# Performance work log

Measured on AMD Instinct MI355X. Metric: run time of the kernel, lower is better.

## Reference

```python
import jax, jax.numpy as jnp
import numpy as np

B, N, DIM = 1, 2048, 2048
H, KVH = 32, 4                 # query heads, kv heads
D = DIM // H                   # head_dim = 64
REP = H // KVH                 # queries per kv = 8
KV_DIM = D * KVH               # 256


def _rope_tables(n, d, base=10000.0):
    inv = 1.0 / (base ** (np.arange(0, d, 2, dtype=np.float32) / d))
    t = np.arange(n, dtype=np.float32)
    freqs = np.outer(t, inv)                      # [n, d/2]
    emb = np.concatenate([freqs, freqs], axis=-1)  # [n, d]
    return jnp.asarray(np.cos(emb)), jnp.asarray(np.sin(emb))


def setup_inputs() -> dict:
    key = jax.random.key(0)
    ks = jax.random.split(key, 5)
    s = 0.02
    cos, sin = _rope_tables(N, D)
    return {
        "x": jax.random.normal(ks[0], (B, N, DIM), jnp.float32),
        "Wq": jax.random.normal(ks[1], (DIM, DIM), jnp.float32) * s,
        "Wk": jax.random.normal(ks[2], (KV_DIM, DIM), jnp.float32) * s,
        "Wv": jax.random.normal(ks[3], (KV_DIM, DIM), jnp.float32) * s,
        "Wo": jax.random.normal(ks[4], (DIM, DIM), jnp.float32) * s,
        "cos": cos,
        "sin": sin,
    }


def _rotate_half(t):
    d2 = t.shape[-1] // 2
    return jnp.concatenate([-t[..., d2:], t[..., :d2]], axis=-1)


def reference(x, Wq, Wk, Wv, Wo, cos, sin):
    b, n, _ = x.shape
    # projections (nn.Linear: x @ W.T)
    q = (x @ Wq.T).reshape(b, n, H, D).transpose(0, 2, 1, 3)     # b h n d
    k = (x @ Wk.T).reshape(b, n, KVH, D).transpose(0, 2, 1, 3)   # b g n d
    v = (x @ Wv.T).reshape(b, n, KVH, D).transpose(0, 2, 1, 3)
    # RoPE
    c = cos[None, None, :, :]
    s = sin[None, None, :, :]
    q = q * c + _rotate_half(q) * s
    k = k * c + _rotate_half(k) * s
    # expand KV heads (repeat_interleave over head dim)
    k = jnp.repeat(k, REP, axis=1)   # b h n d
    v = jnp.repeat(v, REP, axis=1)
    # causal attention with materialized scores (faithful to source)
    scale = 1.0 / jnp.sqrt(jnp.asarray(D, x.dtype))
    scores = jnp.einsum('bhld,bhsd->bhls', q, k) * scale
    causal = jnp.tril(jnp.ones((n, n), bool))
    scores = jnp.where(causal[None, None], scores, jnp.asarray(-jnp.inf, x.dtype))
    attn = jax.nn.softmax(scores, axis=-1)
    y = jnp.einsum('bhls,bhsd->bhld', attn, v)       # b h n d
    y = y.transpose(0, 2, 1, 3).reshape(b, n, DIM)   # b n (h d)
    return y @ Wo.T
```

## Files before the change

kernel.cpp:

```cpp
#include <hip/hip_runtime.h>

typedef unsigned short u16;
typedef __attribute__((ext_vector_type(8))) short short8;
typedef __attribute__((ext_vector_type(4))) float floatx4;

#define N_TOK 2048
#define DIM   2048
#define NH    32
#define NKVH  4
#define HD    64
#define KVD   256

__device__ __forceinline__ float bf2f(u16 u) {
  union { unsigned i; float f; } c; c.i = ((unsigned)u) << 16; return c.f;
}
__device__ __forceinline__ u16 f2bf(float f) {
  union { float f; unsigned i; } c; c.f = f;
  unsigned x = c.i;
  return (u16)((x + 0x7fffu + ((x >> 16) & 1u)) >> 16);
}

__device__ __forceinline__ void gload16(const u16* g, u16* l) {
#if defined(__has_builtin) && __has_builtin(__builtin_amdgcn_global_load_lds)
  __builtin_amdgcn_global_load_lds(
      (const __attribute__((address_space(1))) void*)g,
      (__attribute__((address_space(3))) void*)l, 16, 0, 0);
#else
  *(short8*)l = *(const short8*)g;
#endif
}

#define C_X  1048576
#define C_WQ 2097152
#define C_WK 2228224
#define C_WV 2359296
#define C_WO 3407872
__global__ __launch_bounds__(256) void cvt_all(const float* __restrict__ x,
                                               const float* __restrict__ wq,
                                               const float* __restrict__ wk,
                                               const float* __restrict__ wv,
                                               const float* __restrict__ wo,
                                               u16* __restrict__ dst) {
  int i = blockIdx.x * 256 + threadIdx.x;
  const float* src; int off;
  if      (i < C_X)  { src = x;  off = 0; }
  else if (i < C_WQ) { src = wq; off = C_X; }
  else if (i < C_WK) { src = wk; off = C_WQ; }
  else if (i < C_WV) { src = wv; off = C_WK; }
  else               { src = wo; off = C_WV; }
  float4 v = ((const float4*)src)[i - off];
  ushort4 o;
  o.x = f2bf(v.x); o.y = f2bf(v.y); o.z = f2bf(v.z); o.w = f2bf(v.w);
  ((ushort4*)dst)[i] = o;
}


__global__ __launch_bounds__(256) void gemm_qkv(const u16* __restrict__ A,
                                                const u16* __restrict__ Wq,
                                                const u16* __restrict__ Wk,
                                                const u16* __restrict__ Wv,
                                                const float* __restrict__ cs,
                                                const float* __restrict__ sn,
                                                u16* __restrict__ Qp,
                                                u16* __restrict__ Kp,
                                                u16* __restrict__ Vp) {
  __shared__ __align__(16) u16 As[64 * 32];
  __shared__ __align__(16) u16 Bs[128 * 32];
  const int tid  = threadIdx.x;
  const int lane = tid & 63;
  const int w    = tid >> 6;
  const int r    = lane & 15, q = lane >> 4;
  const int tm = blockIdx.x & 31;
  const int tn = blockIdx.x >> 5;
  const int wm = w & 1, wn = w >> 1;
  const int K = DIM;

  const u16* W; int wrow0;
  if (tn < 16)      { W = Wq; wrow0 = tn * 128; }
  else if (tn < 18) { W = Wk; wrow0 = (tn - 16) * 128; }
  else              { W = Wv; wrow0 = (tn - 18) * 128; }

  const int srow = tid >> 2;
  const int scol = (tid & 3) * 8;
  const u16* ga = A + (size_t)(tm * 64 + srow) * K + scol;
  const u16* gb = W + (size_t)(wrow0 + srow) * K + scol;
  u16* lA = &As[tid * 8];
  u16* lB = &Bs[tid * 8];

  floatx4 acc[2][4];
#pragma unroll
  for (int a = 0; a < 2; ++a)
#pragma unroll
    for (int b = 0; b < 4; ++b) acc[a][b] = (floatx4){0.f, 0.f, 0.f, 0.f};

  for (int k0 = 0; k0 < K; k0 += 32) {
    __syncthreads();
    gload16(ga + k0, lA);
    gload16(gb + k0, lB);
    gload16(gb + k0 + (size_t)64 * K, lB + 2048);
    __syncthreads();

    short8 af[2], bf[4];
#pragma unroll
    for (int mi = 0; mi < 2; ++mi)
      af[mi] = *(const short8*)&As[(wm * 32 + mi * 16 + r) * 32 + q * 8];
#pragma unroll
    for (int nj = 0; nj < 4; ++nj)
      bf[nj] = *(const short8*)&Bs[(wn * 64 + nj * 16 + r) * 32 + q * 8];
#pragma unroll
    for (int mi = 0; mi < 2; ++mi)
#pragma unroll
      for (int nj = 0; nj < 4; ++nj)
        acc[mi][nj] = __builtin_amdgcn_mfma_f32_16x16x32_bf16(af[mi], bf[nj], acc[mi][nj], 0, 0, 0);
  }

  if (tn < 18) {
    const int head = (tn < 16) ? (tn * 2 + wn) : ((tn - 16) * 2 + wn);
#pragma unroll
    for (int mi = 0; mi < 2; ++mi)
#pragma unroll
      for (int g = 0; g < 4; ++g) {
        int row = tm * 64 + wm * 32 + mi * 16 + 4 * q + g;
        const float* crow  = cs + (size_t)row * 64;
        const float* srow2 = sn + (size_t)row * 64;
#pragma unroll
        for (int nj = 0; nj < 2; ++nj) {
          int d = nj * 16 + r;
          float x0 = acc[mi][nj][g];
          float x1 = acc[mi][nj + 2][g];
          float o0 = x0 * crow[d]      - x1 * srow2[d];
          float o1 = x1 * crow[d + 32] + x0 * srow2[d + 32];
          int qq = d >> 3, j = d & 7;
          int lslot = (qq * 16 + (row & 15)) * 8 + j;
          if (tn < 16) {
            int sq = row >> 5, ii = (row >> 4) & 1;
            size_t base = ((size_t)(head * 64 + sq) * 4 + ii * 2) * 512 + lslot;
            Qp[base]       = f2bf(o0);
            Qp[base + 512] = f2bf(o1);
          } else {
            int kt = row >> 6, t = (row >> 4) & 3;
            size_t base = ((size_t)(head * 32 + kt) * 8 + t * 2) * 512 + lslot;
            Kp[base]       = f2bf(o0);
            Kp[base + 512] = f2bf(o1);
          }
        }
      }
  } else {
#pragma unroll
    for (int mi = 0; mi < 2; ++mi)
#pragma unroll
      for (int nj = 0; nj < 4; ++nj) {
        int col  = (tn - 18) * 128 + wn * 64 + nj * 16 + r;
        int kvh  = col >> 6;
        int t    = (col & 63) >> 4;
        int rr   = col & 15;
        int row0 = tm * 64 + wm * 32 + mi * 16 + 4 * q;
        int kt   = row0 >> 6;
        int wk   = row0 & 63;
        int s    = wk >> 5;
        int qq   = (wk & 31) >> 3;
        int j0   = wk & 7;
        uint2 pk;
        pk.x = (unsigned)f2bf(acc[mi][nj][0]) | ((unsigned)f2bf(acc[mi][nj][1]) << 16);
        pk.y = (unsigned)f2bf(acc[mi][nj][2]) | ((unsigned)f2bf(acc[mi][nj][3]) << 16);
        size_t idx = ((size_t)(kvh * 32 + kt) * 8 + s * 4 + t) * 512 + (qq * 16 + rr) * 8 + j0;
        *(uint2*)(Vp + idx) = pk;
      }
  }
}

__global__ __launch_bounds__(256) void gemm_out(const u16* __restrict__ A,
                                                const u16* __restrict__ W,
                                                float* __restrict__ C) {
  __shared__ __align__(16) u16 As[64 * 32];
  __shared__ __align__(16) u16 Bs[128 * 32];
  const int tid  = threadIdx.x;
  const int lane = tid & 63;
  const int w    = tid >> 6;
  const int r    = lane & 15, q = lane >> 4;
  const int tn = blockIdx.x & 15;
  const int tm = blockIdx.x >> 4;
  const int wm = w & 1, wn = w >> 1;
  const int K = DIM;

  const int srow = tid >> 2;
  const int scol = (tid & 3) * 8;
  const u16* ga = A + (size_t)(tm * 64 + srow) * K + scol;
  const u16* gb = W + (size_t)(tn * 128 + srow) * K + scol;
  u16* lA = &As[tid * 8];
  u16* lB = &Bs[tid * 8];

  floatx4 acc[2][4];
#pragma unroll
  for (int a = 0; a < 2; ++a)
#pragma unroll
    for (int b = 0; b < 4; ++b) acc[a][b] = (floatx4){0.f, 0.f, 0.f, 0.f};

  for (int k0 = 0; k0 < K; k0 += 32) {
    __syncthreads();
    gload16(ga + k0, lA);
    gload16(gb + k0, lB);
    gload16(gb + k0 + (size_t)64 * K, lB + 2048);
    __syncthreads();

    short8 af[2], bf[4];
#pragma unroll
    for (int mi = 0; mi < 2; ++mi)
      af[mi] = *(const short8*)&As[(wm * 32 + mi * 16 + r) * 32 + q * 8];
#pragma unroll
    for (int nj = 0; nj < 4; ++nj)
      bf[nj] = *(const short8*)&Bs[(wn * 64 + nj * 16 + r) * 32 + q * 8];
#pragma unroll
    for (int mi = 0; mi < 2; ++mi)
#pragma unroll
      for (int nj = 0; nj < 4; ++nj)
        acc[mi][nj] = __builtin_amdgcn_mfma_f32_16x16x32_bf16(af[mi], bf[nj], acc[mi][nj], 0, 0, 0);
  }

#pragma unroll
  for (int mi = 0; mi < 2; ++mi)
#pragma unroll
    for (int g = 0; g < 4; ++g) {
      int row = tm * 64 + wm * 32 + mi * 16 + 4 * q + g;
#pragma unroll
      for (int nj = 0; nj < 4; ++nj)
        C[(size_t)row * DIM + tn * 128 + wn * 64 + nj * 16 + r] = acc[mi][nj][g];
    }
}

__global__ __launch_bounds__(64, 2) void attn_mfma(const u16* __restrict__ Qp,
                                                   const u16* __restrict__ Kp,
                                                   const u16* __restrict__ Vp,
                                                   u16* __restrict__ Yb) {
  __shared__ __align__(16) u16 Pl[32][72];
  const int lane = threadIdx.x;
  const int r    = lane & 15;
  const int q    = lane >> 4;
  const int bx   = blockIdx.x;
  const int qt   = 15 - (bx >> 2);
  const int sub  = 3 - (bx & 3);
  const int h    = blockIdx.y;
  const int kvh  = h >> 3;
  const int baseq = qt * 128 + sub * 32;
  const int sq   = baseq >> 5;
  const int ktmax = (baseq + 31) >> 6;

  short8 qf[2][2];
#pragma unroll
  for (int i = 0; i < 2; ++i)
#pragma unroll
    for (int c = 0; c < 2; ++c)
      qf[i][c] = *(const short8*)(Qp + ((size_t)(h * 64 + sq) * 4 + i * 2 + c) * 512 + lane * 8);

  floatx4 O[2][4];
  float lsum[2];
#pragma unroll
  for (int i = 0; i < 2; ++i) {
    lsum[i] = 0.f;
#pragma unroll
    for (int t = 0; t < 4; ++t) O[i][t] = (floatx4){0.f, 0.f, 0.f, 0.f};
  }

  const u16* Kbase = Kp + (size_t)(kvh * 32) * 8 * 512;
  const u16* Vbase = Vp + (size_t)(kvh * 32) * 8 * 512;

  auto loadK = [&](int kt, short8 (&kf)[4][2]) {
    const u16* kb = Kbase + (size_t)kt * 8 * 512 + lane * 8;
#pragma unroll
    for (int t = 0; t < 4; ++t) {
      kf[t][0] = *(const short8*)(kb + (t * 2 + 0) * 512);
      kf[t][1] = *(const short8*)(kb + (t * 2 + 1) * 512);
    }
  };

  auto body = [&](int kt, short8 (&kc)[4][2], short8 (&kn)[4][2]) {
    short8 vb[2][4];
    {
      const u16* vbp = Vbase + (size_t)kt * 8 * 512 + lane * 8;
#pragma unroll
      for (int s = 0; s < 2; ++s)
#pragma unroll
        for (int t = 0; t < 4; ++t)
          vb[s][t] = *(const short8*)(vbp + (s * 4 + t) * 512);
    }

    loadK(kt < ktmax ? kt + 1 : ktmax, kn);

    floatx4 ST[2][4];
#pragma unroll
    for (int i = 0; i < 2; ++i)
#pragma unroll
      for (int t = 0; t < 4; ++t) ST[i][t] = (floatx4){0.f, 0.f, 0.f, 0.f};
#pragma unroll
    for (int t = 0; t < 4; ++t)
#pragma unroll
      for (int i = 0; i < 2; ++i) {
        ST[i][t] = __builtin_amdgcn_mfma_f32_16x16x32_bf16(kc[t][0], qf[i][0], ST[i][t], 0, 0, 0);
        ST[i][t] = __builtin_amdgcn_mfma_f32_16x16x32_bf16(kc[t][1], qf[i][1], ST[i][t], 0, 0, 0);
      }

    if (kt == ktmax) {
#pragma unroll
      for (int i = 0; i < 2; ++i) {
        int qrow = baseq + 16 * i + r;
#pragma unroll
        for (int t = 0; t < 4; ++t) {
          int key = kt * 64 + 16 * t + 4 * q;
#pragma unroll
          for (int g = 0; g < 4; ++g)
            if (key + g > qrow) ST[i][t][g] = -1e30f;
        }
      }
    }

#pragma unroll
    for (int i = 0; i < 2; ++i)
#pragma unroll
      for (int t = 0; t < 4; ++t) {
        float p0 = __expf(0.125f * ST[i][t][0]);
        float p1 = __expf(0.125f * ST[i][t][1]);
        float p2 = __expf(0.125f * ST[i][t][2]);
        float p3 = __expf(0.125f * ST[i][t][3]);
        lsum[i] += (p0 + p1) + (p2 + p3);
        uint2 pk;
        pk.x = (unsigned)f2bf(p0) | ((unsigned)f2bf(p1) << 16);
        pk.y = (unsigned)f2bf(p2) | ((unsigned)f2bf(p3) << 16);
        *(uint2*)&Pl[16 * i + r][16 * t + 4 * q] = pk;
      }

#pragma unroll
    for (int s = 0; s < 2; ++s)
#pragma unroll
      for (int i = 0; i < 2; ++i) {
        short8 pa = *(const short8*)&Pl[16 * i + r][32 * s + 8 * q];
#pragma unroll
        for (int t = 0; t < 4; ++t)
          O[i][t] = __builtin_amdgcn_mfma_f32_16x16x32_bf16(pa, vb[s][t], O[i][t], 0, 0, 0);
      }
  };

  short8 kA[4][2], kB[4][2];
  loadK(0, kA);
  for (int kt = 0; kt <= ktmax; kt += 2) {
    body(kt, kA, kB);
    if (kt + 1 <= ktmax) body(kt + 1, kB, kA);
  }

#pragma unroll
  for (int i = 0; i < 2; ++i) {
    lsum[i] += __shfl_xor(lsum[i], 16);
    lsum[i] += __shfl_xor(lsum[i], 32);
  }

#pragma unroll
  for (int i = 0; i < 2; ++i) {
    float inv[4];
#pragma unroll
    for (int g = 0; g < 4; ++g)
      inv[g] = 1.f / __shfl(lsum[i], 4 * q + g);
#pragma unroll
    for (int g = 0; g < 4; ++g) {
      u16* yp = Yb + (size_t)(baseq + 16 * i + 4 * q + g) * DIM + h * 64 + r;
      yp[0]  = f2bf(O[i][0][g] * inv[g]);
      yp[16] = f2bf(O[i][1][g] * inv[g]);
      yp[32] = f2bf(O[i][2][g] * inv[g]);
      yp[48] = f2bf(O[i][3][g] * inv[g]);
    }
  }
}

extern "C" void kernel_launch(void* const* d_in, const int* in_sizes, int n_in,
                              void* d_out, int out_size, void* d_ws, size_t ws_size,
                              hipStream_t stream) {
  const float* x  = (const float*)d_in[0];
  const float* Wq = (const float*)d_in[1];
  const float* Wk = (const float*)d_in[2];
  const float* Wv = (const float*)d_in[3];
  const float* Wo = (const float*)d_in[4];
  const float* cs = (const float*)d_in[5];
  const float* sn = (const float*)d_in[6];

  u16* ws  = (u16*)d_ws;
  u16* xb  = ws;
  u16* Wqb = xb  + (size_t)N_TOK * DIM;
  u16* Wkb = Wqb + (size_t)DIM * DIM;
  u16* Wvb = Wkb + (size_t)KVD * DIM;
  u16* Wob = Wvb + (size_t)KVD * DIM;
  u16* Qp  = Wob + (size_t)DIM * DIM;
  u16* Kp  = Qp  + (size_t)N_TOK * DIM;
  u16* Vp  = Kp  + (size_t)N_TOK * KVD;
  u16* Yb  = Vp  + (size_t)N_TOK * KVD;

  cvt_all<<<dim3(13312), 256, 0, stream>>>(x, Wq, Wk, Wv, Wo, ws);

  gemm_qkv<<<dim3(640), 256, 0, stream>>>(xb, Wqb, Wkb, Wvb, cs, sn, Qp, Kp, Vp);

  attn_mfma<<<dim3(64, 32), 64, 0, stream>>>(Qp, Kp, Vp, Yb);

  gemm_out<<<dim3(512), 256, 0, stream>>>(Yb, Wob, (float*)d_out);
}
```

Before: 226.3 us.

## Enlarge GEMM tiles, split-K output projection, and share K/V tiles via LDS in attention

Both projection GEMMs move from 64x128 to 128x128 block tiles, which halves the grid and raises per-wave MFMA reuse. The output GEMM is split-K in two, writes bf16 partials into the reused x buffer, and a new combine kernel sums them to fp32. Attention now runs four waves per block covering a 128-query tile, staging K/V tiles into double-buffered LDS shared by all waves instead of each wave loading from global. This trades extra partial-sum traffic, a bf16 rounding of the partials, and block-level syncs with causal imbalance across waves for better data reuse.

```diff
diff --git a/kernel.cpp b/kernel.cpp
--- a/kernel.cpp
+++ b/kernel.cpp
@@ -64,14 +64,14 @@
                                                 u16* __restrict__ Qp,
                                                 u16* __restrict__ Kp,
                                                 u16* __restrict__ Vp) {
-  __shared__ __align__(16) u16 As[64 * 32];
+  __shared__ __align__(16) u16 As[128 * 32];
   __shared__ __align__(16) u16 Bs[128 * 32];
   const int tid  = threadIdx.x;
   const int lane = tid & 63;
   const int w    = tid >> 6;
   const int r    = lane & 15, q = lane >> 4;
-  const int tm = blockIdx.x & 31;
-  const int tn = blockIdx.x >> 5;
+  const int tm = blockIdx.x & 15;
+  const int tn = blockIdx.x >> 4;
   const int wm = w & 1, wn = w >> 1;
   const int K = DIM;
 
@@ -80,35 +80,36 @@
   else if (tn < 18) { W = Wk; wrow0 = (tn - 16) * 128; }
   else              { W = Wv; wrow0 = (tn - 18) * 128; }
 
-  const int srow = tid >> 2;
-  const int scol = (tid & 3) * 8;
-  const u16* ga = A + (size_t)(tm * 64 + srow) * K + scol;
+  const int srow = w * 16 + (lane >> 2);
+  const int scol = (lane & 3) * 8;
+  const u16* ga = A + (size_t)(tm * 128 + srow) * K + scol;
   const u16* gb = W + (size_t)(wrow0 + srow) * K + scol;
-  u16* lA = &As[tid * 8];
-  u16* lB = &Bs[tid * 8];
-
-  floatx4 acc[2][4];
-#pragma unroll
-  for (int a = 0; a < 2; ++a)
+  u16* lA = &As[w * 512 + lane * 8];
+  u16* lB = &Bs[w * 512 + lane * 8];
+
+  floatx4 acc[4][4];
+#pragma unroll
+  for (int a = 0; a < 4; ++a)
 #pragma unroll
     for (int b = 0; b < 4; ++b) acc[a][b] = (floatx4){0.f, 0.f, 0.f, 0.f};
 
   for (int k0 = 0; k0 < K; k0 += 32) {
     __syncthreads();
     gload16(ga + k0, lA);
+    gload16(ga + k0 + (size_t)64 * K, lA + 2048);
     gload16(gb + k0, lB);
     gload16(gb + k0 + (size_t)64 * K, lB + 2048);
     __syncthreads();
 
-    short8 af[2], bf[4];
-#pragma unroll
-    for (int mi = 0; mi < 2; ++mi)
-      af[mi] = *(const short8*)&As[(wm * 32 + mi * 16 + r) * 32 + q * 8];
+    short8 af[4], bf[4];
+#pragma unroll
+    for (int mi = 0; mi < 4; ++mi)
+      af[mi] = *(const short8*)&As[(wm * 64 + mi * 16 + r) * 32 + q * 8];
 #pragma unroll
     for (int nj = 0; nj < 4; ++nj)
       bf[nj] = *(const short8*)&Bs[(wn * 64 + nj * 16 + r) * 32 + q * 8];
 #pragma unroll
-    for (int mi = 0; mi < 2; ++mi)
+    for (int mi = 0; mi < 4; ++mi)
 #pragma unroll
       for (int nj = 0; nj < 4; ++nj)
         acc[mi][nj] = __builtin_amdgcn_mfma_f32_16x16x32_bf16(af[mi], bf[nj], acc[mi][nj], 0, 0, 0);
@@ -117,10 +118,10 @@
   if (tn < 18) {
     const int head = (tn < 16) ? (tn * 2 + wn) : ((tn - 16) * 2 + wn);
 #pragma unroll
-    for (int mi = 0; mi < 2; ++mi)
+    for (int mi = 0; mi < 4; ++mi)
 #pragma unroll
       for (int g = 0; g < 4; ++g) {
-        int row = tm * 64 + wm * 32 + mi * 16 + 4 * q + g;
+        int row = tm * 128 + wm * 64 + mi * 16 + 4 * q + g;
         const float* crow  = cs + (size_t)row * 64;
         const float* srow2 = sn + (size_t)row * 64;
 #pragma unroll
@@ -147,14 +148,14 @@
       }
   } else {
 #pragma unroll
-    for (int mi = 0; mi < 2; ++mi)
+    for (int mi = 0; mi < 4; ++mi)
 #pragma unroll
       for (int nj = 0; nj < 4; ++nj) {
         int col  = (tn - 18) * 128 + wn * 64 + nj * 16 + r;
         int kvh  = col >> 6;
         int t    = (col & 63) >> 4;
         int rr   = col & 15;
-        int row0 = tm * 64 + wm * 32 + mi * 16 + 4 * q;
+        int row0 = tm * 128 + wm * 64 + mi * 16 + 4 * q;
         int kt   = row0 >> 6;
         int wk   = row0 & 63;
         int s    = wk >> 5;
@@ -171,8 +172,8 @@
 
 __global__ __launch_bounds__(256) void gemm_out(const u16* __restrict__ A,
                                                 const u16* __restrict__ W,
-                                                float* __restrict__ C) {
-  __shared__ __align__(16) u16 As[64 * 32];
+                                                u16* __restrict__ Pb) {
+  __shared__ __align__(16) u16 As[128 * 32];
   __shared__ __align__(16) u16 Bs[128 * 32];
   const int tid  = threadIdx.x;
   const int lane = tid & 63;
@@ -180,77 +181,105 @@
   const int r    = lane & 15, q = lane >> 4;
   const int tn = blockIdx.x & 15;
   const int tm = blockIdx.x >> 4;
+  const int z  = blockIdx.y;
   const int wm = w & 1, wn = w >> 1;
   const int K = DIM;
 
-  const int srow = tid >> 2;
-  const int scol = (tid & 3) * 8;
-  const u16* ga = A + (size_t)(tm * 64 + srow) * K + scol;
+  const int srow = w * 16 + (lane >> 2);
+  const int scol = (lane & 3) * 8;
+  const u16* ga = A + (size_t)(tm * 128 + srow) * K + scol;
   const u16* gb = W + (size_t)(tn * 128 + srow) * K + scol;
-  u16* lA = &As[tid * 8];
-  u16* lB = &Bs[tid * 8];
-
-  floatx4 acc[2][4];
-#pragma unroll
-  for (int a = 0; a < 2; ++a)
+  u16* lA = &As[w * 512 + lane * 8];
+  u16* lB = &Bs[w * 512 + lane * 8];
+
+  floatx4 acc[4][4];
+#pragma unroll
+  for (int a = 0; a < 4; ++a)
 #pragma unroll
     for (int b = 0; b < 4; ++b) acc[a][b] = (floatx4){0.f, 0.f, 0.f, 0.f};
 
-  for (int k0 = 0; k0 < K; k0 += 32) {
+  const int kbeg = z * 1024, kend = kbeg + 1024;
+  for (int k0 = kbeg; k0 < kend; k0 += 32) {
     __syncthreads();
     gload16(ga + k0, lA);
+    gload16(ga + k0 + (size_t)64 * K, lA + 2048);
     gload16(gb + k0, lB);
     gload16(gb + k0 + (size_t)64 * K, lB + 2048);
     __syncthreads();
 
-    short8 af[2], bf[4];
-#pragma unroll
-    for (int mi = 0; mi < 2; ++mi)
-      af[mi] = *(const short8*)&As[(wm * 32 + mi * 16 + r) * 32 + q * 8];
+    short8 af[4], bf[4];
+#pragma unroll
+    for (int mi = 0; mi < 4; ++mi)
+      af[mi] = *(const short8*)&As[(wm * 64 + mi * 16 + r) * 32 + q * 8];
 #pragma unroll
     for (int nj = 0; nj < 4; ++nj)
       bf[nj] = *(const short8*)&Bs[(wn * 64 + nj * 16 + r) * 32 + q * 8];
 #pragma unroll
-    for (int mi = 0; mi < 2; ++mi)
+    for (int mi = 0; mi < 4; ++mi)
 #pragma unroll
       for (int nj = 0; nj < 4; ++nj)
         acc[mi][nj] = __builtin_amdgcn_mfma_f32_16x16x32_bf16(af[mi], bf[nj], acc[mi][nj], 0, 0, 0);
   }
 
-#pragma unroll
-  for (int mi = 0; mi < 2; ++mi)
+  u16* P = Pb + (size_t)z * N_TOK * DIM;
+#pragma unroll
+  for (int mi = 0; mi < 4; ++mi)
 #pragma unroll
     for (int g = 0; g < 4; ++g) {
-      int row = tm * 64 + wm * 32 + mi * 16 + 4 * q + g;
+      int row = tm * 128 + wm * 64 + mi * 16 + 4 * q + g;
 #pragma unroll
       for (int nj = 0; nj < 4; ++nj)
-        C[(size_t)row * DIM + tn * 128 + wn * 64 + nj * 16 + r] = acc[mi][nj][g];
+        P[(size_t)row * DIM + tn * 128 + wn * 64 + nj * 16 + r] = f2bf(acc[mi][nj][g]);
     }
 }
 
-__global__ __launch_bounds__(64, 2) void attn_mfma(const u16* __restrict__ Qp,
-                                                   const u16* __restrict__ Kp,
-                                                   const u16* __restrict__ Vp,
-                                                   u16* __restrict__ Yb) {
-  __shared__ __align__(16) u16 Pl[32][72];
-  const int lane = threadIdx.x;
+__global__ __launch_bounds__(256) void combine_out(const u16* __restrict__ Pb,
+                                                   float* __restrict__ out) {
+  int idx = blockIdx.x * 256 + threadIdx.x;
+  const short8 a = *(const short8*)(Pb + (size_t)idx * 8);
+  const short8 b = *(const short8*)(Pb + (size_t)N_TOK * DIM + (size_t)idx * 8);
+  float4 o0, o1;
+  o0.x = bf2f((u16)a[0]) + bf2f((u16)b[0]);
+  o0.y = bf2f((u16)a[1]) + bf2f((u16)b[1]);
+  o0.z = bf2f((u16)a[2]) + bf2f((u16)b[2]);
+  o0.w = bf2f((u16)a[3]) + bf2f((u16)b[3]);
+  o1.x = bf2f((u16)a[4]) + bf2f((u16)b[4]);
+  o1.y = bf2f((u16)a[5]) + bf2f((u16)b[5]);
+  o1.z = bf2f((u16)a[6]) + bf2f((u16)b[6]);
+  o1.w = bf2f((u16)a[7]) + bf2f((u16)b[7]);
+  ((float4*)out)[idx * 2]     = o0;
+  ((float4*)out)[idx * 2 + 1] = o1;
+}
+
+__global__ __launch_bounds__(256) void attn_mfma(const u16* __restrict__ Qp,
+                                                 const u16* __restrict__ Kp,
+                                                 const u16* __restrict__ Vp,
+                                                 u16* __restrict__ Yb) {
+  __shared__ __align__(16) u16 Kbuf[2][8 * 512];
+  __shared__ __align__(16) u16 Vbuf[2][8 * 512];
+  __shared__ __align__(16) u16 Pl[4][32][72];
+  const int tid  = threadIdx.x;
+  const int lane = tid & 63;
+  const int w    = tid >> 6;
   const int r    = lane & 15;
   const int q    = lane >> 4;
-  const int bx   = blockIdx.x;
-  const int qt   = 15 - (bx >> 2);
-  const int sub  = 3 - (bx & 3);
+  const int qt   = 15 - blockIdx.x;
   const int h    = blockIdx.y;
   const int kvh  = h >> 3;
-  const int baseq = qt * 128 + sub * 32;
-  const int sq   = baseq >> 5;
-  const int ktmax = (baseq + 31) >> 6;
+  const int baseq = qt * 128 + w * 32;
+  const int ktmax_blk = 2 * qt + 1;
+  const int ktmax_w   = (baseq + 31) >> 6;
+
+  const u16* Kg = Kp + (size_t)(kvh * 32) * 4096;
+  const u16* Vg = Vp + (size_t)(kvh * 32) * 4096;
 
   short8 qf[2][2];
 #pragma unroll
   for (int i = 0; i < 2; ++i)
 #pragma unroll
     for (int c = 0; c < 2; ++c)
-      qf[i][c] = *(const short8*)(Qp + ((size_t)(h * 64 + sq) * 4 + i * 2 + c) * 512 + lane * 8);
+      qf[i][c] = *(const short8*)(Qp +
+          ((size_t)(h * 64 + qt * 4 + w) * 4 + i * 2 + c) * 512 + lane * 8);
 
   floatx4 O[2][4];
   float lsum[2];
@@ -261,89 +290,85 @@
     for (int t = 0; t < 4; ++t) O[i][t] = (floatx4){0.f, 0.f, 0.f, 0.f};
   }
 
-  const u16* Kbase = Kp + (size_t)(kvh * 32) * 8 * 512;
-  const u16* Vbase = Vp + (size_t)(kvh * 32) * 8 * 512;
-
-  auto loadK = [&](int kt, short8 (&kf)[4][2]) {
-    const u16* kb = Kbase + (size_t)kt * 8 * 512 + lane * 8;
-#pragma unroll
-    for (int t = 0; t < 4; ++t) {
-      kf[t][0] = *(const short8*)(kb + (t * 2 + 0) * 512);
-      kf[t][1] = *(const short8*)(kb + (t * 2 + 1) * 512);
-    }
+  auto stage = [&](int kt, int buf) {
+    const u16* src = ((w < 2) ? Kg : Vg) + (size_t)kt * 4096;
+    u16* dst = (w < 2) ? &Kbuf[buf][0] : &Vbuf[buf][0];
+    const int f0 = (w & 1) * 4;
+#pragma unroll
+    for (int j = 0; j < 4; ++j)
+      gload16(src + (f0 + j) * 512 + lane * 8, dst + (f0 + j) * 512 + lane * 8);
   };
 
-  auto body = [&](int kt, short8 (&kc)[4][2], short8 (&kn)[4][2]) {
-    short8 vb[2][4];
-    {
-      const u16* vbp = Vbase + (size_t)kt * 8 * 512 + lane * 8;
-#pragma unroll
-      for (int s = 0; s < 2; ++s)
+  stage(0, 0);
+  __syncthreads();
+
+  for (int kt = 0; kt <= ktmax_blk; ++kt) {
+    const int buf = kt & 1;
+    if (kt < ktmax_blk) stage(kt + 1, buf ^ 1);
+
+    if (kt <= ktmax_w) {
+      floatx4 ST[2][4];
+#pragma unroll
+      for (int i = 0; i < 2; ++i)
+#pragma unroll
+        for (int t = 0; t < 4; ++t) ST[i][t] = (floatx4){0.f, 0.f, 0.f, 0.f};
+#pragma unroll
+      for (int t = 0; t < 4; ++t) {
+        short8 kf0 = *(const short8*)&Kbuf[buf][(t * 2 + 0) * 512 + lane * 8];
+        short8 kf1 = *(const short8*)&Kbuf[buf][(t * 2 + 1) * 512 + lane * 8];
+#pragma unroll
+        for (int i = 0; i < 2; ++i) {
+          ST[i][t] = __builtin_amdgcn_mfma_f32_16x16x32_bf16(kf0, qf[i][0], ST[i][t], 0, 0, 0);
+          ST[i][t] = __builtin_amdgcn_mfma_f32_16x16x32_bf16(kf1, qf[i][1], ST[i][t], 0, 0, 0);
+        }
+      }
+
+      if (kt == ktmax_w) {
+#pragma unroll
+        for (int i = 0; i < 2; ++i) {
+          int qrow = baseq + 16 * i + r;
+#pragma unroll
+          for (int t = 0; t < 4; ++t) {
+            int key = kt * 64 + 16 * t + 4 * q;
+#pragma unroll
+            for (int g = 0; g < 4; ++g)
+              if (key + g > qrow) ST[i][t][g] = -1e30f;
+          }
+        }
+      }
+
+#pragma unroll
+      for (int i = 0; i < 2; ++i)
+#pragma unroll
+        for (int t = 0; t < 4; ++t) {
+          float p0 = __expf(0.125f * ST[i][t][0]);
+          float p1 = __expf(0.125f * ST[i][t][1]);
+          float p2 = __expf(0.125f * ST[i][t][2]);
+          float p3 = __expf(0.125f * ST[i][t][3]);
+          lsum[i] += (p0 + p1) + (p2 + p3);
+          uint2 pk;
+          pk.x = (unsigned)f2bf(p0) | ((unsigned)f2bf(p1) << 16);
+          pk.y = (unsigned)f2bf(p2) | ((unsigned)f2bf(p3) << 16);
+          *(uint2*)&Pl[w][16 * i + r][16 * t + 4 * q] = pk;
+        }
+
+#pragma unroll
+      for (int s = 0; s < 2; ++s) {
+        short8 vb[4];
 #pragma unroll
         for (int t = 0; t < 4; ++t)
-          vb[s][t] = *(const short8*)(vbp + (s * 4 + t) * 512);
-    }
-
-    loadK(kt < ktmax ? kt + 1 : ktmax, kn);
-
-    floatx4 ST[2][4];
-#pragma unroll
-    for (int i = 0; i < 2; ++i)
-#pragma unroll
-      for (int t = 0; t < 4; ++t) ST[i][t] = (floatx4){0.f, 0.f, 0.f, 0.f};
-#pragma unroll
-    for (int t = 0; t < 4; ++t)
-#pragma unroll
-      for (int i = 0; i < 2; ++i) {
-        ST[i][t] = __builtin_amdgcn_mfma_f32_16x16x32_bf16(kc[t][0], qf[i][0], ST[i][t], 0, 0, 0);
-        ST[i][t] = __builtin_amdgcn_mfma_f32_16x16x32_bf16(kc[t][1], qf[i][1], ST[i][t], 0, 0, 0);
-      }
-
-    if (kt == ktmax) {
-#pragma unroll
-      for (int i = 0; i < 2; ++i) {
-        int qrow = baseq + 16 * i + r;
-#pragma unroll
-        for (int t = 0; t < 4; ++t) {
-          int key = kt * 64 + 16 * t + 4 * q;
-#pragma unroll
-          for (int g = 0; g < 4; ++g)
-            if (key + g > qrow) ST[i][t][g] = -1e30f;
+          vb[t] = *(const short8*)&Vbuf[buf][(s * 4 + t) * 512 + lane * 8];
+#pragma unroll
+        for (int i = 0; i < 2; ++i) {
+          short8 pa = *(const short8*)&Pl[w][16 * i + r][32 * s + 8 * q];
+#pragma unroll
+          for (int t = 0; t < 4; ++t)
+            O[i][t] = __builtin_amdgcn_mfma_f32_16x16x32_bf16(pa, vb[t], O[i][t], 0, 0, 0);
         }
       }
     }
 
-#pragma unroll
-    for (int i = 0; i < 2; ++i)
-#pragma unroll
-      for (int t = 0; t < 4; ++t) {
-        float p0 = __expf(0.125f * ST[i][t][0]);
-        float p1 = __expf(0.125f * ST[i][t][1]);
-        float p2 = __expf(0.125f * ST[i][t][2]);
-        float p3 = __expf(0.125f * ST[i][t][3]);
-        lsum[i] += (p0 + p1) + (p2 + p3);
-        uint2 pk;
-        pk.x = (unsigned)f2bf(p0) | ((unsigned)f2bf(p1) << 16);
-        pk.y = (unsigned)f2bf(p2) | ((unsigned)f2bf(p3) << 16);
-        *(uint2*)&Pl[16 * i + r][16 * t + 4 * q] = pk;
-      }
-
-#pragma unroll
-    for (int s = 0; s < 2; ++s)
-#pragma unroll
-      for (int i = 0; i < 2; ++i) {
-        short8 pa = *(const short8*)&Pl[16 * i + r][32 * s + 8 * q];
-#pragma unroll
-        for (int t = 0; t < 4; ++t)
-          O[i][t] = __builtin_amdgcn_mfma_f32_16x16x32_bf16(pa, vb[s][t], O[i][t], 0, 0, 0);
-      }
-  };
-
-  short8 kA[4][2], kB[4][2];
-  loadK(0, kA);
-  for (int kt = 0; kt <= ktmax; kt += 2) {
-    body(kt, kA, kB);
-    if (kt + 1 <= ktmax) body(kt + 1, kB, kA);
+    __syncthreads();
   }
 
 #pragma unroll
@@ -391,11 +416,15 @@
   u16* Vp  = Kp  + (size_t)N_TOK * KVD;
   u16* Yb  = Vp  + (size_t)N_TOK * KVD;
 
+  u16* Pb  = xb;
+
   cvt_all<<<dim3(13312), 256, 0, stream>>>(x, Wq, Wk, Wv, Wo, ws);
 
-  gemm_qkv<<<dim3(640), 256, 0, stream>>>(xb, Wqb, Wkb, Wvb, cs, sn, Qp, Kp, Vp);
-
-  attn_mfma<<<dim3(64, 32), 64, 0, stream>>>(Qp, Kp, Vp, Yb);
-
-  gemm_out<<<dim3(512), 256, 0, stream>>>(Yb, Wob, (float*)d_out);
-}
+  gemm_qkv<<<dim3(320), 256, 0, stream>>>(xb, Wqb, Wkb, Wvb, cs, sn, Qp, Kp, Vp);
+
+  attn_mfma<<<dim3(16, 32), 256, 0, stream>>>(Qp, Kp, Vp, Yb);
+
+  gemm_out<<<dim3(256, 2), 256, 0, stream>>>(Yb, Wob, Pb);
+
+  combine_out<<<dim3(2048), 256, 0, stream>>>(Pb, (float*)d_out);
+}
```

After: 249.3 us. 1.1x slower.
